# Kernel tuning notes

Hardware: AMD Instinct MI355X
Metric: run time of the kernel (lower is better)

## Reference

```python
import jax, jax.numpy as jnp
import numpy as np
from jax import lax

BN_EPS = 1e-5


def _conv(x, w, b, stride):
    # x: [N,C,H,W], w: [O,I,3,3], stride 2, padding 1
    y = lax.conv_general_dilated(
        x, w, window_strides=(stride, stride), padding=((1, 1), (1, 1)),
        dimension_numbers=('NCHW', 'OIHW', 'NCHW'))
    return y + b[None, :, None, None]


def _batchnorm(x, gamma, beta):
    # training-mode BN: batch statistics over (N,H,W)
    mean = jnp.mean(x, axis=(0, 2, 3), keepdims=True)
    var = jnp.var(x, axis=(0, 2, 3), keepdims=True)
    xn = (x - mean) * lax.rsqrt(var + BN_EPS)
    return xn * gamma[None, :, None, None] + beta[None, :, None, None]


def _maxpool2(x):
    return lax.reduce_window(x, -jnp.inf, lax.max, (1, 1, 2, 2), (1, 1, 2, 2), 'VALID')


def setup_inputs() -> dict:
    key = jax.random.key(0)
    ks = jax.random.split(key, 8)
    B, C, H, W = 128, 3, 224, 224
    x = jax.random.normal(ks[0], (B, C, H, W), dtype=jnp.float32)
    conv1_w = jax.random.normal(ks[1], (16, 3, 3, 3), dtype=jnp.float32) * (1.0 / np.sqrt(3 * 9))
    conv1_b = jnp.zeros((16,), dtype=jnp.float32)
    bn1_g = jnp.ones((16,), dtype=jnp.float32)
    bn1_b = jnp.zeros((16,), dtype=jnp.float32)
    conv2_w = jax.random.normal(ks[2], (32, 16, 3, 3), dtype=jnp.float32) * (1.0 / np.sqrt(16 * 9))
    conv2_b = jnp.zeros((32,), dtype=jnp.float32)
    bn2_g = jnp.ones((32,), dtype=jnp.float32)
    bn2_b = jnp.zeros((32,), dtype=jnp.float32)
    fc_w = jax.random.normal(ks[3], (1, 32), dtype=jnp.float32) * (1.0 / np.sqrt(32))
    fc_b = jnp.zeros((1,), dtype=jnp.float32)
    return dict(x=x, conv1_w=conv1_w, conv1_b=conv1_b, bn1_g=bn1_g, bn1_b=bn1_b,
                conv2_w=conv2_w, conv2_b=conv2_b, bn2_g=bn2_g, bn2_b=bn2_b,
                fc_w=fc_w, fc_b=fc_b)


def reference(x, conv1_w, conv1_b, bn1_g, bn1_b, conv2_w, conv2_b, bn2_g, bn2_b, fc_w, fc_b):
    h = jax.nn.relu(_batchnorm(_conv(x, conv1_w, conv1_b, 2), bn1_g, bn1_b))   # [B,16,112,112]
    h = _maxpool2(h)                                                           # [B,16,56,56]
    h = jax.nn.relu(_batchnorm(_conv(h, conv2_w, conv2_b, 2), bn2_g, bn2_b))   # [B,32,28,28]
    h = jnp.mean(h, axis=(2, 3))                                               # AdaptiveAvgPool2d((1,1)) -> [B,32]
    logits = h @ fc_w.T + fc_b                                                 # [B,1]
    # Quantum circuit: RY(theta) on all wires, CNOT chain, <Z_0>.
    # Z on the control wire commutes with every CNOT -> expval = cos(theta).
    probs = jnp.cos(logits)                                                    # [B,1]
    return jnp.concatenate((probs, 1.0 - probs), axis=-1)                      # [B,2]
```

## Files before the change

### kernel.cpp

```cpp
#include <hip/hip_runtime.h>
#include <math.h>

#define BATCH 128
#define CIN 3
#define H 224
#define W 224
#define C1 16
#define HP 56
#define WP 56
#define C2 32
#define H2 28
#define W2 28

#define TROWS 17
#define CHF (TROWS * W)
#define CHB (CHF * 4)

__global__ __launch_bounds__(256) void conv1_fused_k(
    const float* __restrict__ x, const float* __restrict__ w1,
    const float* __restrict__ b1, float2* __restrict__ mm,
    float* __restrict__ s_sum, float* __restrict__ s_sq)
{
    __shared__ __align__(16) float tile[3 * CHF];
    __shared__ float red[4][16], redq[4][16];

    const int tid = threadIdx.x;
    const int wave = tid >> 6, lane = tid & 63;
    const int bid = blockIdx.x;
    const int n = bid / 14;
    const int g = bid % 14;
    const int ph0 = g * 4;
    const int ph = ph0 + wave;
    const int pw = (lane < 56) ? lane : 55;
    const bool active = lane < 56;
    const bool topok = ph > 0;
    const bool pwok  = pw > 0;

    const int startrow = (g == 0) ? 0 : (4 * ph0 - 1);
    const int nops     = (g == 0) ? 14 : 15;
    const int base_off = (g == 0) ? (W * 4) : 0;
#pragma unroll
    for (int ci = 0; ci < CIN; ++ci) {
        const char* gch = (const char*)(x + ((size_t)n * CIN + ci) * (H * W)
                                        + (size_t)startrow * W);
        char* lch = (char*)tile + ci * CHB + base_off;
        for (int kp = wave; kp < nops; kp += 4) {
            int off = kp * 1024;
            if (off > 14208) off = 14208;
            __builtin_amdgcn_global_load_lds(
                (const __attribute__((address_space(1))) void*)(gch + off + lane * 16),
                (__attribute__((address_space(3))) void*)(lch + off),
                16, 0, 0);
        }
    }

    float acc[16][4];
#pragma unroll
    for (int j = 0; j < 16; ++j) {
        const float bb = b1[j];
#pragma unroll
        for (int q = 0; q < 4; ++q) acc[j][q] = bb;
    }

    __syncthreads();

#pragma unroll
    for (int ci = 0; ci < CIN; ++ci) {
#pragma unroll
        for (int l = 0; l < 5; ++l) {
            const int tr = 4 * wave + l;
            const float* rp = tile + ci * CHF + tr * W;
            const float4 fa = *(const float4*)(rp + 4 * pw);
            const float4 fb = *(const float4*)(rp + max(4 * pw - 4, 0));
            const bool rok = (l > 0) || topok;
            const float p0 = (rok && pwok) ? fb.w : 0.0f;
            const float p1 = rok ? fa.x : 0.0f;
            const float p2 = rok ? fa.y : 0.0f;
            const float p3 = rok ? fa.z : 0.0f;
            const float p4 = rok ? fa.w : 0.0f;
#pragma unroll
            for (int j = 0; j < 16; ++j) {
                const float* wc = w1 + (j * CIN + ci) * 9;
                if (l < 3) {
                    const float wa = wc[l * 3 + 0];
                    const float wb = wc[l * 3 + 1];
                    const float wd = wc[l * 3 + 2];
                    acc[j][0] += wa * p0 + wb * p1 + wd * p2;
                    acc[j][1] += wa * p2 + wb * p3 + wd * p4;
                }
                if (l >= 2) {
                    const int kh = l - 2;
                    const float wa = wc[kh * 3 + 0];
                    const float wb = wc[kh * 3 + 1];
                    const float wd = wc[kh * 3 + 2];
                    acc[j][2] += wa * p0 + wb * p1 + wd * p2;
                    acc[j][3] += wa * p2 + wb * p3 + wd * p4;
                }
            }
        }
    }

#pragma unroll
    for (int j = 0; j < 16; ++j) {
        const float a0 = acc[j][0], a1 = acc[j][1], a2 = acc[j][2], a3 = acc[j][3];
        if (active) {
            const int o = (n * C1 + j) * (HP * WP) + ph * WP + pw;
            mm[o] = make_float2(fmaxf(fmaxf(a0, a1), fmaxf(a2, a3)),
                                fminf(fminf(a0, a1), fminf(a2, a3)));
        }
        float s = active ? (a0 + a1 + a2 + a3) : 0.0f;
        float q = active ? (a0 * a0 + a1 * a1 + a2 * a2 + a3 * a3) : 0.0f;
#pragma unroll
        for (int off = 32; off > 0; off >>= 1) {
            s += __shfl_xor(s, off);
            q += __shfl_xor(q, off);
        }
        if (lane == 0) { red[wave][j] = s; redq[wave][j] = q; }
    }
    __syncthreads();
    if (tid < 16) {
        atomicAdd(&s_sum[tid],
                  red[0][tid] + red[1][tid] + red[2][tid] + red[3][tid]);
    } else if (tid < 32) {
        const int j = tid - 16;
        atomicAdd(&s_sq[j],
                  redq[0][j] + redq[1][j] + redq[2][j] + redq[3][j]);
    }
}

__global__ __launch_bounds__(256) void conv2_k(
    const float2* __restrict__ mm,
    const float* __restrict__ s1sum, const float* __restrict__ s1sq,
    const float* __restrict__ g1, const float* __restrict__ be1,
    const float* __restrict__ w2, const float* __restrict__ b2,
    float* __restrict__ y2,
    float* __restrict__ s_sum, float* __restrict__ s_sq)
{
    __shared__ float red[4][8], redq[4][8];
    const int tid = threadIdx.x;
    const int t = blockIdx.x * 256 + tid;
    const int c0 = blockIdx.y * 8;
    const int n = t / 392;
    const int r = t % 392;
    const int oh = r / 14;
    const int ow = (r % 14) * 2;
    const bool topok = oh > 0;
    const bool owok  = ow > 0;
    const float inv1 = 1.0f / (float)(BATCH * 112 * 112);

    float accA[8], accB[8];
#pragma unroll
    for (int c = 0; c < 8; ++c) { accA[c] = b2[c0 + c]; accB[c] = accA[c]; }

#pragma unroll 2
    for (int ci = 0; ci < C1; ++ci) {
        const float mean = s1sum[ci] * inv1;
        const float var  = s1sq[ci] * inv1 - mean * mean;
        const float s1 = g1[ci] * rsqrtf(var + 1e-5f);
        const float t1 = be1[ci] - mean * s1;

        const float2* pl = mm + (n * C1 + ci) * (HP * WP);

        float4 fa[3], fb[3];
        float2 lpv[3];
#pragma unroll
        for (int kh = 0; kh < 3; ++kh) {
            const int ih = max(2 * oh - 1 + kh, 0);
            const float2* rowp = pl + ih * WP;
            fa[kh]  = *(const float4*)(rowp + 2 * ow);
            fb[kh]  = *(const float4*)(rowp + 2 * ow + 2);
            lpv[kh] = rowp[max(2 * ow - 1, 0)];
        }

        float h[3][5];
#pragma unroll
        for (int kh = 0; kh < 3; ++kh) {
            const bool rok = (kh > 0) || topok;
            const float u0 = fmaxf(0.0f, fmaxf(s1 * lpv[kh].x + t1, s1 * lpv[kh].y + t1));
            const float u1 = fmaxf(0.0f, fmaxf(s1 * fa[kh].x + t1, s1 * fa[kh].y + t1));
            const float u2 = fmaxf(0.0f, fmaxf(s1 * fa[kh].z + t1, s1 * fa[kh].w + t1));
            const float u3 = fmaxf(0.0f, fmaxf(s1 * fb[kh].x + t1, s1 * fb[kh].y + t1));
            const float u4 = fmaxf(0.0f, fmaxf(s1 * fb[kh].z + t1, s1 * fb[kh].w + t1));
            h[kh][0] = (rok && owok) ? u0 : 0.0f;
            h[kh][1] = rok ? u1 : 0.0f;
            h[kh][2] = rok ? u2 : 0.0f;
            h[kh][3] = rok ? u3 : 0.0f;
            h[kh][4] = rok ? u4 : 0.0f;
        }

#pragma unroll
        for (int c = 0; c < 8; ++c) {
            const float* wc = w2 + ((c0 + c) * C1 + ci) * 9;
            float a = accA[c], b = accB[c];
#pragma unroll
            for (int kh = 0; kh < 3; ++kh) {
                const float w0 = wc[kh * 3 + 0];
                const float w1v = wc[kh * 3 + 1];
                const float w2v = wc[kh * 3 + 2];
                a += w0 * h[kh][0] + w1v * h[kh][1] + w2v * h[kh][2];
                b += w0 * h[kh][2] + w1v * h[kh][3] + w2v * h[kh][4];
            }
            accA[c] = a; accB[c] = b;
        }
    }

#pragma unroll
    for (int c = 0; c < 8; ++c) {
        const float aA = accA[c], aB = accB[c];
        const int p = oh * W2 + ow;
        *(float2*)(y2 + (n * C2 + c0 + c) * (H2 * W2) + p) = make_float2(aA, aB);
        float s = aA + aB, q = aA * aA + aB * aB;
#pragma unroll
        for (int off = 32; off > 0; off >>= 1) {
            s += __shfl_xor(s, off);
            q += __shfl_xor(q, off);
        }
        if ((tid & 63) == 0) { red[tid >> 6][c] = s; redq[tid >> 6][c] = q; }
    }
    __syncthreads();
    if (tid < 8) {
        atomicAdd(&s_sum[c0 + tid],
                  red[0][tid] + red[1][tid] + red[2][tid] + red[3][tid]);
    } else if (tid < 16) {
        const int c = tid - 8;
        atomicAdd(&s_sq[c0 + c],
                  redq[0][c] + redq[1][c] + redq[2][c] + redq[3][c]);
    }
}

__global__ __launch_bounds__(256) void head_fused_k(
    const float* __restrict__ y2,
    const float* __restrict__ s2sum, const float* __restrict__ s2sq,
    const float* __restrict__ g2, const float* __restrict__ be2,
    const float* __restrict__ fcw, const float* __restrict__ fcb,
    float* __restrict__ out)
{
    __shared__ float feat[C2];
    const int n = blockIdx.x;
    const int tid = threadIdx.x;
    const int wave = tid >> 6, lane = tid & 63;
    const float inv2 = 1.0f / (float)(BATCH * H2 * W2);
#pragma unroll
    for (int k = 0; k < 8; ++k) {
        const int c = wave * 8 + k;
        const float mean = s2sum[c] * inv2;
        const float var  = s2sq[c] * inv2 - mean * mean;
        const float s = g2[c] * rsqrtf(var + 1e-5f);
        const float t = be2[c] - mean * s;
        const float4* yp = (const float4*)(y2 + (n * C2 + c) * (H2 * W2));
        float a = 0.0f;
        for (int i = lane; i < 196; i += 64) {
            const float4 v = yp[i];
            a += fmaxf(0.0f, s * v.x + t) + fmaxf(0.0f, s * v.y + t)
               + fmaxf(0.0f, s * v.z + t) + fmaxf(0.0f, s * v.w + t);
        }
#pragma unroll
        for (int off = 32; off > 0; off >>= 1) a += __shfl_xor(a, off);
        if (lane == 0) feat[c] = a * (1.0f / (H2 * W2));
    }
    __syncthreads();
    if (tid == 0) {
        float logit = fcb[0];
#pragma unroll
        for (int c = 0; c < C2; ++c) logit += feat[c] * fcw[c];
        const float pc = cosf(logit);
        out[2 * n]     = pc;
        out[2 * n + 1] = 1.0f - pc;
    }
}

extern "C" void kernel_launch(void* const* d_in, const int* in_sizes, int n_in,
                              void* d_out, int out_size, void* d_ws, size_t ws_size,
                              hipStream_t stream) {
    const float* x   = (const float*)d_in[0];
    const float* w1  = (const float*)d_in[1];
    const float* b1  = (const float*)d_in[2];
    const float* g1  = (const float*)d_in[3];
    const float* be1 = (const float*)d_in[4];
    const float* w2  = (const float*)d_in[5];
    const float* b2  = (const float*)d_in[6];
    const float* g2  = (const float*)d_in[7];
    const float* be2 = (const float*)d_in[8];
    const float* fcw = (const float*)d_in[9];
    const float* fcb = (const float*)d_in[10];
    float* out = (float*)d_out;

    float* ws = (float*)d_ws;
    float2* mm = (float2*)ws;
    float* y2 = ws + (size_t)2 * BATCH * C1 * HP * WP;
    float* stats = y2 + (size_t)BATCH * C2 * H2 * W2;
    float* s1sum = stats;
    float* s1sq  = stats + 16;
    float* s2sum = stats + 32;
    float* s2sq  = stats + 64;

    hipMemsetAsync(stats, 0, 96 * sizeof(float), stream);

    conv1_fused_k<<<dim3(1792), 256, 0, stream>>>(x, w1, b1, mm, s1sum, s1sq);
    conv2_k<<<dim3(196, 4), 256, 0, stream>>>(mm, s1sum, s1sq, g1, be1,
                                              w2, b2, y2, s2sum, s2sq);
    head_fused_k<<<BATCH, 256, 0, stream>>>(y2, s2sum, s2sq, g2, be2,
                                            fcw, fcb, out);
}
```

Before: 219.8 us.

## Fuse conv1, conv2 and head into one cooperative persistent kernel with grid syncs

Replaces the memset plus three separate kernel launches with a single cooperative kernel. Blocks loop persistently over the conv1, conv2 and head work items, and grid.sync separates the batch-statistic phases. The stats buffer is zeroed inside the kernel. This removes launch gaps and the memset, but adds grid-wide barriers, caps the grid at the occupancy limit, and may lower occupancy because the kernel now holds more registers and shared memory.

```diff
diff --git a/kernel.cpp b/kernel.cpp
--- a/kernel.cpp
+++ b/kernel.cpp
@@ -1,5 +1,8 @@
 #include <hip/hip_runtime.h>
+#include <hip/hip_cooperative_groups.h>
 #include <math.h>
+
+namespace cg = cooperative_groups;
 
 #define BATCH 128
 #define CIN 3
@@ -16,256 +19,268 @@
 #define CHF (TROWS * W)
 #define CHB (CHF * 4)
 
-__global__ __launch_bounds__(256) void conv1_fused_k(
+__global__ __launch_bounds__(256) void fused_all_k(
     const float* __restrict__ x, const float* __restrict__ w1,
-    const float* __restrict__ b1, float2* __restrict__ mm,
-    float* __restrict__ s_sum, float* __restrict__ s_sq)
+    const float* __restrict__ b1, const float* __restrict__ g1,
+    const float* __restrict__ be1, const float* __restrict__ w2,
+    const float* __restrict__ b2, const float* __restrict__ g2,
+    const float* __restrict__ be2, const float* __restrict__ fcw,
+    const float* __restrict__ fcb, float2* __restrict__ mm,
+    float* __restrict__ y2, float* __restrict__ stats,
+    float* __restrict__ out)
 {
+    cg::grid_group grid = cg::this_grid();
     __shared__ __align__(16) float tile[3 * CHF];
     __shared__ float red[4][16], redq[4][16];
+    __shared__ float feat[C2];
+
+    float* s1sum = stats;
+    float* s1sq  = stats + 16;
+    float* s2sum = stats + 32;
+    float* s2sq  = stats + 64;
 
     const int tid = threadIdx.x;
     const int wave = tid >> 6, lane = tid & 63;
-    const int bid = blockIdx.x;
-    const int n = bid / 14;
-    const int g = bid % 14;
-    const int ph0 = g * 4;
-    const int ph = ph0 + wave;
-    const int pw = (lane < 56) ? lane : 55;
-    const bool active = lane < 56;
-    const bool topok = ph > 0;
-    const bool pwok  = pw > 0;
-
-    const int startrow = (g == 0) ? 0 : (4 * ph0 - 1);
-    const int nops     = (g == 0) ? 14 : 15;
-    const int base_off = (g == 0) ? (W * 4) : 0;
-#pragma unroll
-    for (int ci = 0; ci < CIN; ++ci) {
-        const char* gch = (const char*)(x + ((size_t)n * CIN + ci) * (H * W)
-                                        + (size_t)startrow * W);
-        char* lch = (char*)tile + ci * CHB + base_off;
-        for (int kp = wave; kp < nops; kp += 4) {
-            int off = kp * 1024;
-            if (off > 14208) off = 14208;
-            __builtin_amdgcn_global_load_lds(
-                (const __attribute__((address_space(1))) void*)(gch + off + lane * 16),
-                (__attribute__((address_space(3))) void*)(lch + off),
-                16, 0, 0);
+
+    if (blockIdx.x == 0 && tid < 96) stats[tid] = 0.0f;
+    __threadfence();
+    grid.sync();
+    __threadfence();
+
+    for (int u = blockIdx.x; u < 1792; u += gridDim.x) {
+        const int n = u / 14;
+        const int g = u % 14;
+        const int ph = g * 4 + wave;
+        const int pw = (lane < 56) ? lane : 55;
+        const bool active = lane < 56;
+        const bool topok = ph > 0;
+        const bool pwok  = pw > 0;
+
+        const int startrow = (g == 0) ? 0 : (16 * g - 1);
+        const int nops     = (g == 0) ? 14 : 15;
+        const int base_off = (g == 0) ? (W * 4) : 0;
+#pragma unroll
+        for (int ci = 0; ci < CIN; ++ci) {
+            const char* gch = (const char*)(x + ((size_t)n * CIN + ci) * (H * W)
+                                            + (size_t)startrow * W);
+            char* lch = (char*)tile + ci * CHB + base_off;
+            for (int kp = wave; kp < nops; kp += 4) {
+                int off = kp * 1024;
+                if (off > 14208) off = 14208;
+                __builtin_amdgcn_global_load_lds(
+                    (const __attribute__((address_space(1))) void*)(gch + off + lane * 16),
+                    (__attribute__((address_space(3))) void*)(lch + off),
+                    16, 0, 0);
+            }
+        }
+
+        float acc[16][4];
+#pragma unroll
+        for (int j = 0; j < 16; ++j) {
+            const float bb = b1[j];
+#pragma unroll
+            for (int q = 0; q < 4; ++q) acc[j][q] = bb;
+        }
+
+        __syncthreads();
+
+#pragma unroll
+        for (int ci = 0; ci < CIN; ++ci) {
+#pragma unroll
+            for (int l = 0; l < 5; ++l) {
+                const int tr = 4 * wave + l;
+                const float* rp = tile + ci * CHF + tr * W;
+                const float4 fa = *(const float4*)(rp + 4 * pw);
+                const float4 fb = *(const float4*)(rp + max(4 * pw - 4, 0));
+                const bool rok = (l > 0) || topok;
+                const float p0 = (rok && pwok) ? fb.w : 0.0f;
+                const float p1 = rok ? fa.x : 0.0f;
+                const float p2 = rok ? fa.y : 0.0f;
+                const float p3 = rok ? fa.z : 0.0f;
+                const float p4 = rok ? fa.w : 0.0f;
+#pragma unroll
+                for (int j = 0; j < 16; ++j) {
+                    const float* wc = w1 + (j * CIN + ci) * 9;
+                    if (l < 3) {
+                        const float wa = wc[l * 3 + 0];
+                        const float wb = wc[l * 3 + 1];
+                        const float wd = wc[l * 3 + 2];
+                        acc[j][0] += wa * p0 + wb * p1 + wd * p2;
+                        acc[j][1] += wa * p2 + wb * p3 + wd * p4;
+                    }
+                    if (l >= 2) {
+                        const int kh = l - 2;
+                        const float wa = wc[kh * 3 + 0];
+                        const float wb = wc[kh * 3 + 1];
+                        const float wd = wc[kh * 3 + 2];
+                        acc[j][2] += wa * p0 + wb * p1 + wd * p2;
+                        acc[j][3] += wa * p2 + wb * p3 + wd * p4;
+                    }
+                }
+            }
+        }
+
+#pragma unroll
+        for (int j = 0; j < 16; ++j) {
+            const float a0 = acc[j][0], a1 = acc[j][1], a2 = acc[j][2], a3 = acc[j][3];
+            if (active) {
+                const int o = (n * C1 + j) * (HP * WP) + ph * WP + pw;
+                mm[o] = make_float2(fmaxf(fmaxf(a0, a1), fmaxf(a2, a3)),
+                                    fminf(fminf(a0, a1), fminf(a2, a3)));
+            }
+            float s = active ? (a0 + a1 + a2 + a3) : 0.0f;
+            float q = active ? (a0 * a0 + a1 * a1 + a2 * a2 + a3 * a3) : 0.0f;
+#pragma unroll
+            for (int off = 32; off > 0; off >>= 1) {
+                s += __shfl_xor(s, off);
+                q += __shfl_xor(q, off);
+            }
+            if (lane == 0) { red[wave][j] = s; redq[wave][j] = q; }
+        }
+        __syncthreads();
+        if (tid < 16) {
+            atomicAdd(&s1sum[tid],
+                      red[0][tid] + red[1][tid] + red[2][tid] + red[3][tid]);
+        } else if (tid < 32) {
+            const int j = tid - 16;
+            atomicAdd(&s1sq[j],
+                      redq[0][j] + redq[1][j] + redq[2][j] + redq[3][j]);
         }
     }
 
-    float acc[16][4];
-#pragma unroll
-    for (int j = 0; j < 16; ++j) {
-        const float bb = b1[j];
-#pragma unroll
-        for (int q = 0; q < 4; ++q) acc[j][q] = bb;
+    __threadfence();
+    grid.sync();
+    __threadfence();
+
+    {
+        const float inv1 = 1.0f / (float)(BATCH * 112 * 112);
+        for (int v = blockIdx.x; v < 784; v += gridDim.x) {
+            const int bx = v % 196, by = v / 196;
+            const int t = bx * 256 + tid;
+            const int c0 = by * 8;
+            const int n = t / 392;
+            const int r = t % 392;
+            const int oh = r / 14;
+            const int ow = (r % 14) * 2;
+            const bool topok = oh > 0;
+            const bool owok  = ow > 0;
+
+            float accA[8], accB[8];
+#pragma unroll
+            for (int c = 0; c < 8; ++c) { accA[c] = b2[c0 + c]; accB[c] = accA[c]; }
+
+#pragma unroll 2
+            for (int ci = 0; ci < C1; ++ci) {
+                const float mean = s1sum[ci] * inv1;
+                const float var  = s1sq[ci] * inv1 - mean * mean;
+                const float s1 = g1[ci] * rsqrtf(var + 1e-5f);
+                const float t1 = be1[ci] - mean * s1;
+
+                const float2* pl = mm + (n * C1 + ci) * (HP * WP);
+
+                float4 fa[3], fb[3];
+                float2 lpv[3];
+#pragma unroll
+                for (int kh = 0; kh < 3; ++kh) {
+                    const int ih = max(2 * oh - 1 + kh, 0);
+                    const float2* rowp = pl + ih * WP;
+                    fa[kh]  = *(const float4*)(rowp + 2 * ow);
+                    fb[kh]  = *(const float4*)(rowp + 2 * ow + 2);
+                    lpv[kh] = rowp[max(2 * ow - 1, 0)];
+                }
+
+                float h[3][5];
+#pragma unroll
+                for (int kh = 0; kh < 3; ++kh) {
+                    const bool rok = (kh > 0) || topok;
+                    const float u0 = fmaxf(0.0f, fmaxf(s1 * lpv[kh].x + t1, s1 * lpv[kh].y + t1));
+                    const float u1 = fmaxf(0.0f, fmaxf(s1 * fa[kh].x + t1, s1 * fa[kh].y + t1));
+                    const float u2 = fmaxf(0.0f, fmaxf(s1 * fa[kh].z + t1, s1 * fa[kh].w + t1));
+                    const float u3 = fmaxf(0.0f, fmaxf(s1 * fb[kh].x + t1, s1 * fb[kh].y + t1));
+                    const float u4 = fmaxf(0.0f, fmaxf(s1 * fb[kh].z + t1, s1 * fb[kh].w + t1));
+                    h[kh][0] = (rok && owok) ? u0 : 0.0f;
+                    h[kh][1] = rok ? u1 : 0.0f;
+                    h[kh][2] = rok ? u2 : 0.0f;
+                    h[kh][3] = rok ? u3 : 0.0f;
+                    h[kh][4] = rok ? u4 : 0.0f;
+                }
+
+#pragma unroll
+                for (int c = 0; c < 8; ++c) {
+                    const float* wc = w2 + ((c0 + c) * C1 + ci) * 9;
+                    float a = accA[c], b = accB[c];
+#pragma unroll
+                    for (int kh = 0; kh < 3; ++kh) {
+                        const float w0 = wc[kh * 3 + 0];
+                        const float w1v = wc[kh * 3 + 1];
+                        const float w2v = wc[kh * 3 + 2];
+                        a += w0 * h[kh][0] + w1v * h[kh][1] + w2v * h[kh][2];
+                        b += w0 * h[kh][2] + w1v * h[kh][3] + w2v * h[kh][4];
+                    }
+                    accA[c] = a; accB[c] = b;
+                }
+            }
+
+#pragma unroll
+            for (int c = 0; c < 8; ++c) {
+                const float aA = accA[c], aB = accB[c];
+                const int p = oh * W2 + ow;
+                *(float2*)(y2 + (n * C2 + c0 + c) * (H2 * W2) + p) = make_float2(aA, aB);
+                float s = aA + aB, q = aA * aA + aB * aB;
+#pragma unroll
+                for (int off = 32; off > 0; off >>= 1) {
+                    s += __shfl_xor(s, off);
+                    q += __shfl_xor(q, off);
+                }
+                if ((tid & 63) == 0) { red[tid >> 6][c] = s; redq[tid >> 6][c] = q; }
+            }
+            __syncthreads();
+            if (tid < 8) {
+                atomicAdd(&s2sum[c0 + tid],
+                          red[0][tid] + red[1][tid] + red[2][tid] + red[3][tid]);
+            } else if (tid < 16) {
+                const int c = tid - 8;
+                atomicAdd(&s2sq[c0 + c],
+                          redq[0][c] + redq[1][c] + redq[2][c] + redq[3][c]);
+            }
+            __syncthreads();
+        }
     }
 
-    __syncthreads();
-
-#pragma unroll
-    for (int ci = 0; ci < CIN; ++ci) {
-#pragma unroll
-        for (int l = 0; l < 5; ++l) {
-            const int tr = 4 * wave + l;
-            const float* rp = tile + ci * CHF + tr * W;
-            const float4 fa = *(const float4*)(rp + 4 * pw);
-            const float4 fb = *(const float4*)(rp + max(4 * pw - 4, 0));
-            const bool rok = (l > 0) || topok;
-            const float p0 = (rok && pwok) ? fb.w : 0.0f;
-            const float p1 = rok ? fa.x : 0.0f;
-            const float p2 = rok ? fa.y : 0.0f;
-            const float p3 = rok ? fa.z : 0.0f;
-            const float p4 = rok ? fa.w : 0.0f;
-#pragma unroll
-            for (int j = 0; j < 16; ++j) {
-                const float* wc = w1 + (j * CIN + ci) * 9;
-                if (l < 3) {
-                    const float wa = wc[l * 3 + 0];
-                    const float wb = wc[l * 3 + 1];
-                    const float wd = wc[l * 3 + 2];
-                    acc[j][0] += wa * p0 + wb * p1 + wd * p2;
-                    acc[j][1] += wa * p2 + wb * p3 + wd * p4;
-                }
-                if (l >= 2) {
-                    const int kh = l - 2;
-                    const float wa = wc[kh * 3 + 0];
-                    const float wb = wc[kh * 3 + 1];
-                    const float wd = wc[kh * 3 + 2];
-                    acc[j][2] += wa * p0 + wb * p1 + wd * p2;
-                    acc[j][3] += wa * p2 + wb * p3 + wd * p4;
-                }
-            }
-        }
-    }
-
-#pragma unroll
-    for (int j = 0; j < 16; ++j) {
-        const float a0 = acc[j][0], a1 = acc[j][1], a2 = acc[j][2], a3 = acc[j][3];
-        if (active) {
-            const int o = (n * C1 + j) * (HP * WP) + ph * WP + pw;
-            mm[o] = make_float2(fmaxf(fmaxf(a0, a1), fmaxf(a2, a3)),
-                                fminf(fminf(a0, a1), fminf(a2, a3)));
-        }
-        float s = active ? (a0 + a1 + a2 + a3) : 0.0f;
-        float q = active ? (a0 * a0 + a1 * a1 + a2 * a2 + a3 * a3) : 0.0f;
-#pragma unroll
-        for (int off = 32; off > 0; off >>= 1) {
-            s += __shfl_xor(s, off);
-            q += __shfl_xor(q, off);
-        }
-        if (lane == 0) { red[wave][j] = s; redq[wave][j] = q; }
-    }
-    __syncthreads();
-    if (tid < 16) {
-        atomicAdd(&s_sum[tid],
-                  red[0][tid] + red[1][tid] + red[2][tid] + red[3][tid]);
-    } else if (tid < 32) {
-        const int j = tid - 16;
-        atomicAdd(&s_sq[j],
-                  redq[0][j] + redq[1][j] + redq[2][j] + redq[3][j]);
-    }
-}
-
-__global__ __launch_bounds__(256) void conv2_k(
-    const float2* __restrict__ mm,
-    const float* __restrict__ s1sum, const float* __restrict__ s1sq,
-    const float* __restrict__ g1, const float* __restrict__ be1,
-    const float* __restrict__ w2, const float* __restrict__ b2,
-    float* __restrict__ y2,
-    float* __restrict__ s_sum, float* __restrict__ s_sq)
-{
-    __shared__ float red[4][8], redq[4][8];
-    const int tid = threadIdx.x;
-    const int t = blockIdx.x * 256 + tid;
-    const int c0 = blockIdx.y * 8;
-    const int n = t / 392;
-    const int r = t % 392;
-    const int oh = r / 14;
-    const int ow = (r % 14) * 2;
-    const bool topok = oh > 0;
-    const bool owok  = ow > 0;
-    const float inv1 = 1.0f / (float)(BATCH * 112 * 112);
-
-    float accA[8], accB[8];
-#pragma unroll
-    for (int c = 0; c < 8; ++c) { accA[c] = b2[c0 + c]; accB[c] = accA[c]; }
-
-#pragma unroll 2
-    for (int ci = 0; ci < C1; ++ci) {
-        const float mean = s1sum[ci] * inv1;
-        const float var  = s1sq[ci] * inv1 - mean * mean;
-        const float s1 = g1[ci] * rsqrtf(var + 1e-5f);
-        const float t1 = be1[ci] - mean * s1;
-
-        const float2* pl = mm + (n * C1 + ci) * (HP * WP);
-
-        float4 fa[3], fb[3];
-        float2 lpv[3];
-#pragma unroll
-        for (int kh = 0; kh < 3; ++kh) {
-            const int ih = max(2 * oh - 1 + kh, 0);
-            const float2* rowp = pl + ih * WP;
-            fa[kh]  = *(const float4*)(rowp + 2 * ow);
-            fb[kh]  = *(const float4*)(rowp + 2 * ow + 2);
-            lpv[kh] = rowp[max(2 * ow - 1, 0)];
-        }
-
-        float h[3][5];
-#pragma unroll
-        for (int kh = 0; kh < 3; ++kh) {
-            const bool rok = (kh > 0) || topok;
-            const float u0 = fmaxf(0.0f, fmaxf(s1 * lpv[kh].x + t1, s1 * lpv[kh].y + t1));
-            const float u1 = fmaxf(0.0f, fmaxf(s1 * fa[kh].x + t1, s1 * fa[kh].y + t1));
-            const float u2 = fmaxf(0.0f, fmaxf(s1 * fa[kh].z + t1, s1 * fa[kh].w + t1));
-            const float u3 = fmaxf(0.0f, fmaxf(s1 * fb[kh].x + t1, s1 * fb[kh].y + t1));
-            const float u4 = fmaxf(0.0f, fmaxf(s1 * fb[kh].z + t1, s1 * fb[kh].w + t1));
-            h[kh][0] = (rok && owok) ? u0 : 0.0f;
-            h[kh][1] = rok ? u1 : 0.0f;
-            h[kh][2] = rok ? u2 : 0.0f;
-            h[kh][3] = rok ? u3 : 0.0f;
-            h[kh][4] = rok ? u4 : 0.0f;
-        }
-
-#pragma unroll
-        for (int c = 0; c < 8; ++c) {
-            const float* wc = w2 + ((c0 + c) * C1 + ci) * 9;
-            float a = accA[c], b = accB[c];
-#pragma unroll
-            for (int kh = 0; kh < 3; ++kh) {
-                const float w0 = wc[kh * 3 + 0];
-                const float w1v = wc[kh * 3 + 1];
-                const float w2v = wc[kh * 3 + 2];
-                a += w0 * h[kh][0] + w1v * h[kh][1] + w2v * h[kh][2];
-                b += w0 * h[kh][2] + w1v * h[kh][3] + w2v * h[kh][4];
-            }
-            accA[c] = a; accB[c] = b;
-        }
-    }
-
-#pragma unroll
-    for (int c = 0; c < 8; ++c) {
-        const float aA = accA[c], aB = accB[c];
-        const int p = oh * W2 + ow;
-        *(float2*)(y2 + (n * C2 + c0 + c) * (H2 * W2) + p) = make_float2(aA, aB);
-        float s = aA + aB, q = aA * aA + aB * aB;
-#pragma unroll
-        for (int off = 32; off > 0; off >>= 1) {
-            s += __shfl_xor(s, off);
-            q += __shfl_xor(q, off);
-        }
-        if ((tid & 63) == 0) { red[tid >> 6][c] = s; redq[tid >> 6][c] = q; }
-    }
-    __syncthreads();
-    if (tid < 8) {
-        atomicAdd(&s_sum[c0 + tid],
-                  red[0][tid] + red[1][tid] + red[2][tid] + red[3][tid]);
-    } else if (tid < 16) {
-        const int c = tid - 8;
-        atomicAdd(&s_sq[c0 + c],
-                  redq[0][c] + redq[1][c] + redq[2][c] + redq[3][c]);
-    }
-}
-
-__global__ __launch_bounds__(256) void head_fused_k(
-    const float* __restrict__ y2,
-    const float* __restrict__ s2sum, const float* __restrict__ s2sq,
-    const float* __restrict__ g2, const float* __restrict__ be2,
-    const float* __restrict__ fcw, const float* __restrict__ fcb,
-    float* __restrict__ out)
-{
-    __shared__ float feat[C2];
-    const int n = blockIdx.x;
-    const int tid = threadIdx.x;
-    const int wave = tid >> 6, lane = tid & 63;
-    const float inv2 = 1.0f / (float)(BATCH * H2 * W2);
-#pragma unroll
-    for (int k = 0; k < 8; ++k) {
-        const int c = wave * 8 + k;
-        const float mean = s2sum[c] * inv2;
-        const float var  = s2sq[c] * inv2 - mean * mean;
-        const float s = g2[c] * rsqrtf(var + 1e-5f);
-        const float t = be2[c] - mean * s;
-        const float4* yp = (const float4*)(y2 + (n * C2 + c) * (H2 * W2));
-        float a = 0.0f;
-        for (int i = lane; i < 196; i += 64) {
-            const float4 v = yp[i];
-            a += fmaxf(0.0f, s * v.x + t) + fmaxf(0.0f, s * v.y + t)
-               + fmaxf(0.0f, s * v.z + t) + fmaxf(0.0f, s * v.w + t);
-        }
-#pragma unroll
-        for (int off = 32; off > 0; off >>= 1) a += __shfl_xor(a, off);
-        if (lane == 0) feat[c] = a * (1.0f / (H2 * W2));
-    }
-    __syncthreads();
-    if (tid == 0) {
-        float logit = fcb[0];
-#pragma unroll
-        for (int c = 0; c < C2; ++c) logit += feat[c] * fcw[c];
-        const float pc = cosf(logit);
-        out[2 * n]     = pc;
-        out[2 * n + 1] = 1.0f - pc;
+    __threadfence();
+    grid.sync();
+    __threadfence();
+
+    for (int n = blockIdx.x; n < BATCH; n += gridDim.x) {
+        const float inv2 = 1.0f / (float)(BATCH * H2 * W2);
+#pragma unroll
+        for (int k = 0; k < 8; ++k) {
+            const int c = wave * 8 + k;
+            const float mean = s2sum[c] * inv2;
+            const float var  = s2sq[c] * inv2 - mean * mean;
+            const float s = g2[c] * rsqrtf(var + 1e-5f);
+            const float t = be2[c] - mean * s;
+            const float4* yp = (const float4*)(y2 + (n * C2 + c) * (H2 * W2));
+            float a = 0.0f;
+            for (int i = lane; i < 196; i += 64) {
+                const float4 v = yp[i];
+                a += fmaxf(0.0f, s * v.x + t) + fmaxf(0.0f, s * v.y + t)
+                   + fmaxf(0.0f, s * v.z + t) + fmaxf(0.0f, s * v.w + t);
+            }
+#pragma unroll
+            for (int off = 32; off > 0; off >>= 1) a += __shfl_xor(a, off);
+            if (lane == 0) feat[c] = a * (1.0f / (H2 * W2));
+        }
+        __syncthreads();
+        if (tid == 0) {
+            float logit = fcb[0];
+#pragma unroll
+            for (int c = 0; c < C2; ++c) logit += feat[c] * fcw[c];
+            const float pc = cosf(logit);
+            out[2 * n]     = pc;
+            out[2 * n + 1] = 1.0f - pc;
+        }
+        __syncthreads();
     }
 }
 
@@ -289,16 +304,24 @@
     float2* mm = (float2*)ws;
     float* y2 = ws + (size_t)2 * BATCH * C1 * HP * WP;
     float* stats = y2 + (size_t)BATCH * C2 * H2 * W2;
-    float* s1sum = stats;
-    float* s1sq  = stats + 16;
-    float* s2sum = stats + 32;
-    float* s2sq  = stats + 64;
-
-    hipMemsetAsync(stats, 0, 96 * sizeof(float), stream);
-
-    conv1_fused_k<<<dim3(1792), 256, 0, stream>>>(x, w1, b1, mm, s1sum, s1sq);
-    conv2_k<<<dim3(196, 4), 256, 0, stream>>>(mm, s1sum, s1sq, g1, be1,
-                                              w2, b2, y2, s2sum, s2sq);
-    head_fused_k<<<BATCH, 256, 0, stream>>>(y2, s2sum, s2sq, g2, be2,
-                                            fcw, fcb, out);
+
+    static int g_grid = 0;
+    if (g_grid == 0) {
+        int nb = 0;
+        hipError_t e = hipOccupancyMaxActiveBlocksPerMultiprocessor(
+            &nb, fused_all_k, 256, 0);
+        if (e != hipSuccess || nb < 1) nb = 2;
+        int gsz = nb * 256;
+        if (gsz > 1792) gsz = 1792;
+        g_grid = gsz;
+    }
+
+    void* args[] = {
+        (void*)&x, (void*)&w1, (void*)&b1, (void*)&g1, (void*)&be1,
+        (void*)&w2, (void*)&b2, (void*)&g2, (void*)&be2,
+        (void*)&fcw, (void*)&fcb,
+        (void*)&mm, (void*)&y2, (void*)&stats, (void*)&out
+    };
+    hipLaunchCooperativeKernel(fused_all_k, dim3(g_grid), dim3(256),
+                               args, 0, stream);
 }
```

New measurement: 518.6 us. 136% more time.
